# Kernel tuning notes

Hardware: AMD Instinct MI355X
Metric: run time of the kernel (lower is better)

## Reference

```python
import jax, jax.numpy as jnp
import numpy as np

B, NS, NF, T, D = 64, 2, 13, 24, 512
H = 8
DH = D // H
DFF = 2048
EPS = 1e-5


def setup_inputs() -> dict:
    key = jax.random.key(0)
    ks = jax.random.split(key, 16)
    s = 0.02
    inp = {
        'x': jax.random.normal(ks[0], (B, NS * NF, T, D), jnp.float32),
        'w_in_s': jax.random.normal(ks[1], (3 * D, D), jnp.float32) * s,
        'b_in_s': jnp.zeros((3 * D,), jnp.float32),
        'w_out_s': jax.random.normal(ks[2], (D, D), jnp.float32) * s,
        'b_out_s': jnp.zeros((D,), jnp.float32),
        'w_in_f': jax.random.normal(ks[3], (3 * D, D), jnp.float32) * s,
        'b_in_f': jnp.zeros((3 * D,), jnp.float32),
        'w_out_f': jax.random.normal(ks[4], (D, D), jnp.float32) * s,
        'b_out_f': jnp.zeros((D,), jnp.float32),
        'w1': jax.random.normal(ks[5], (DFF, D), jnp.float32) * s,
        'b1': jnp.zeros((DFF,), jnp.float32),
        'w2': jax.random.normal(ks[6], (D, DFF), jnp.float32) * s,
        'b2': jnp.zeros((D,), jnp.float32),
        'g1': jnp.ones((D,), jnp.float32), 'be1': jnp.zeros((D,), jnp.float32),
        'g2': jnp.ones((D,), jnp.float32), 'be2': jnp.zeros((D,), jnp.float32),
        'g3': jnp.ones((D,), jnp.float32), 'be3': jnp.zeros((D,), jnp.float32),
    }
    return inp


def _layer_norm(x, g, b):
    mu = jnp.mean(x, axis=-1, keepdims=True)
    var = jnp.mean(jnp.square(x - mu), axis=-1, keepdims=True)
    return (x - mu) * jax.lax.rsqrt(var + EPS) * g + b


def _mha(x, w_in, b_in, w_out, b_out):
    # x: [..., S, D]; torch nn.MultiheadAttention math, eval mode (no dropout)
    qkv = x @ w_in.T + b_in                     # [..., S, 3D]
    q, k, v = jnp.split(qkv, 3, axis=-1)
    shp = q.shape[:-1] + (H, DH)
    q, k, v = q.reshape(shp), k.reshape(shp), v.reshape(shp)
    scores = jnp.einsum('...qhd,...khd->...hqk', q, k) / np.sqrt(DH).astype(np.float32)
    a = jax.nn.softmax(scores, axis=-1)
    o = jnp.einsum('...hqk,...khd->...qhd', a, v).reshape(x.shape)
    return o @ w_out.T + b_out


def reference(x, w_in_s, b_in_s, w_out_s, b_out_s, w_in_f, b_in_f, w_out_f, b_out_f,
              w1, b1, w2, b2, g1, be1, g2, be2, g3, be3):
    xr = x.reshape(B, NS, NF, T, D)
    # station attention: attend over the NS axis for each (feature, t)
    xs = xr.transpose(0, 2, 3, 1, 4)            # [B, NF, T, NS, D]
    xs = xs + _mha(xs, w_in_s, b_in_s, w_out_s, b_out_s)
    x = xs.transpose(0, 3, 1, 2, 4).reshape(B, NS * NF, T, D)
    x = _layer_norm(x, g1, be1)
    # feature attention: attend over the NF axis for each (station, t)
    xr = x.reshape(B, NS, NF, T, D)
    xf = xr.transpose(0, 1, 3, 2, 4)            # [B, NS, T, NF, D]
    xf = xf + _mha(xf, w_in_f, b_in_f, w_out_f, b_out_f)
    x = xf.transpose(0, 1, 3, 2, 4).reshape(B, NS * NF, T, D)
    x = _layer_norm(x, g2, be2)
    # feed-forward
    ff = jax.nn.relu(x @ w1.T + b1) @ w2.T + b2
    x = _layer_norm(x + ff, g3, be3)
    return x
```

## Files before the change

kernel.cpp:

```cpp
#include <hip/hip_runtime.h>
#include <stdint.h>

typedef unsigned short u16;
typedef __bf16 bf16x8 __attribute__((ext_vector_type(8)));
typedef float f32x4 __attribute__((ext_vector_type(4)));

#define DEV __device__ __forceinline__

DEV float bf2f(u16 u) {
    union { uint32_t u; float f; } c; c.u = ((uint32_t)u) << 16; return c.f;
}
DEV u16 f2bf(float f) {
    union { float f; uint32_t u; } c; c.f = f;
    uint32_t u = c.u;
    u += 0x7FFFu + ((u >> 16) & 1u);
    return (u16)(u >> 16);
}

DEV void gload_lds16(const u16* gp, u16* lp) {
    __builtin_amdgcn_global_load_lds(
        (__attribute__((address_space(1))) u16*)(uintptr_t)gp,
        (__attribute__((address_space(3))) u16*)lp,
        16, 0, 0);
}

#define WAITVM6 asm volatile("s_waitcnt vmcnt(6)" ::: "memory")
#define WAITVM4 asm volatile("s_waitcnt vmcnt(4)" ::: "memory")
#define WAITVM0 asm volatile("s_waitcnt vmcnt(0)" ::: "memory")
#define MEMFENCE asm volatile("" ::: "memory")

DEV void load16f(const u16* p, float* f) {
    uint4 a = *reinterpret_cast<const uint4*>(p);
    uint4 b = *reinterpret_cast<const uint4*>(p + 8);
    uint32_t w[8] = { a.x, a.y, a.z, a.w, b.x, b.y, b.z, b.w };
#pragma unroll
    for (int k = 0; k < 8; ++k) {
        union { uint32_t u; float f; } lo, hi;
        lo.u = w[k] << 16; hi.u = w[k] & 0xFFFF0000u;
        f[2 * k] = lo.f; f[2 * k + 1] = hi.f;
    }
}
DEV float dot16(const u16* p, const float* q) {
    uint4 a = *reinterpret_cast<const uint4*>(p);
    uint4 b = *reinterpret_cast<const uint4*>(p + 8);
    uint32_t w[8] = { a.x, a.y, a.z, a.w, b.x, b.y, b.z, b.w };
    float d = 0.0f;
#pragma unroll
    for (int k = 0; k < 8; ++k) {
        union { uint32_t u; float f; } lo, hi;
        lo.u = w[k] << 16; hi.u = w[k] & 0xFFFF0000u;
        d += q[2 * k] * lo.f;
        d += q[2 * k + 1] * hi.f;
    }
    return d;
}
DEV void fma16(const u16* p, float pw, float* acc) {
    uint4 a = *reinterpret_cast<const uint4*>(p);
    uint4 b = *reinterpret_cast<const uint4*>(p + 8);
    uint32_t w[8] = { a.x, a.y, a.z, a.w, b.x, b.y, b.z, b.w };
#pragma unroll
    for (int k = 0; k < 8; ++k) {
        union { uint32_t u; float f; } lo, hi;
        lo.u = w[k] << 16; hi.u = w[k] & 0xFFFF0000u;
        acc[2 * k] += pw * lo.f;
        acc[2 * k + 1] += pw * hi.f;
    }
}
DEV void store16(u16* p, const float* y) {
    uint32_t w[8];
#pragma unroll
    for (int k = 0; k < 8; ++k)
        w[k] = (uint32_t)f2bf(y[2 * k]) | ((uint32_t)f2bf(y[2 * k + 1]) << 16);
    uint4 a = { w[0], w[1], w[2], w[3] };
    uint4 b = { w[4], w[5], w[6], w[7] };
    *reinterpret_cast<uint4*>(p) = a;
    *reinterpret_cast<uint4*>(p + 8) = b;
}

__global__ __launch_bounds__(256) void k_f32_to_bf16(
    const float* __restrict__ in, u16* __restrict__ out, int n4)
{
    int i = blockIdx.x * 256 + threadIdx.x;
    if (i >= n4) return;
    float4 v = reinterpret_cast<const float4*>(in)[i];
    ushort4 o;
    o.x = f2bf(v.x); o.y = f2bf(v.y); o.z = f2bf(v.z); o.w = f2bf(v.w);
    reinterpret_cast<ushort4*>(out)[i] = o;
}

template<bool RELU, bool RESID, int NT>
__global__ __launch_bounds__(512, 2) void k_gemm8p(
    const u16* __restrict__ A, const u16* __restrict__ W,
    const float* __restrict__ bias, const u16* __restrict__ res,
    u16* __restrict__ C, int M, int N, int K)
{
    __shared__ __align__(16) u16 Abuf[2][16384];
    __shared__ __align__(16) u16 Bbuf[2][16384];

    const int tid  = threadIdx.x;
    const int lane = tid & 63;
    const int wave = tid >> 6;
    const int wm   = wave >> 2;
    const int wn   = wave & 3;
    const int l15  = lane & 15;
    const int lg   = lane >> 4;

    const int nwg = gridDim.x;
    const int v = (blockIdx.x & 7) * (nwg >> 3) + (blockIdx.x >> 3);
    const long tileM = (long)(v / NT) * 256;
    const long tileN = (long)(v % NT) * 256;

    const int nIter = K >> 7;

    f32x4 acc[8][4] = {};

    const long Abase = (tileM + (tid >> 3)) * (long)K + (((tid & 7) ^ ((tid >> 3) & 7)) << 3);
    const long Bbase = (tileN + (tid >> 3)) * (long)K + (((tid & 7) ^ ((tid >> 3) & 7)) << 3);

    auto stA = [&](int h, int t) {
#pragma unroll
        for (int e = 0; e < 2; ++e)
            gload_lds16(A + Abase + (long)(h * 128 + e * 64) * K + t * 64,
                        &Abuf[t & 1][(h * 1024 + e * 512 + tid) * 8]);
    };
    auto stB = [&](int h, int t) {
#pragma unroll
        for (int e = 0; e < 2; ++e)
            gload_lds16(W + Bbase + (long)(h * 128 + e * 64) * K + t * 64,
                        &Bbuf[t & 1][(h * 1024 + e * 512 + tid) * 8]);
    };

    int koff[2];
#pragma unroll
    for (int ks = 0; ks < 2; ++ks)
        koff[ks] = ((ks * 4 + lg) ^ (l15 & 7)) * 8;
    const int aRow = wm * 128 + l15;
    const int bRow = wn * 64 + l15;

    stA(0, 0); stA(1, 0); stB(0, 0); stB(1, 0); stB(0, 1); stB(1, 1);
    WAITVM4;
    MEMFENCE;
    __builtin_amdgcn_s_barrier();
    MEMFENCE;

    bf16x8 b[4][2];

    for (int j = 0; j < nIter; ++j) {
        const bool pre = (j + 1 < nIter);
        const int E = 2 * j;
#pragma unroll
        for (int ph = 0; ph < 8; ++ph) {
            const int bb = ph >> 2;
            const int q  = ph & 3;
            if (q == 0) {
#pragma unroll
                for (int n = 0; n < 4; ++n)
#pragma unroll
                    for (int ks = 0; ks < 2; ++ks)
                        b[n][ks] = *reinterpret_cast<const bf16x8*>(
                            &Bbuf[bb][(bRow + n * 16) * 64 + koff[ks]]);
            }
            bf16x8 aq[2][2];
#pragma unroll
            for (int mi = 0; mi < 2; ++mi)
#pragma unroll
                for (int ks = 0; ks < 2; ++ks)
                    aq[mi][ks] = *reinterpret_cast<const bf16x8*>(
                        &Abuf[bb][(aRow + (q * 2 + mi) * 16) * 64 + koff[ks]]);
            if (ph == 0) stA(0, E + 1);
            else if (ph == 1) stA(1, E + 1);
            else if (ph == 2) { if (pre) stB(0, E + 2); }
            else if (ph == 3) {
                if (pre) { stB(1, E + 2); WAITVM4; } else { WAITVM0; }
            }
            else if (ph == 4) { if (pre) stA(0, E + 2); }
            else if (ph == 5) { if (pre) stA(1, E + 2); }
            else if (ph == 6) { if (pre) stB(0, E + 3); }
            else {
                if (pre) { stB(1, E + 3); WAITVM4; } else { WAITVM0; }
            }
            MEMFENCE;
            __builtin_amdgcn_s_barrier();
            MEMFENCE;
            __builtin_amdgcn_s_setprio(1);
#pragma unroll
            for (int mi = 0; mi < 2; ++mi)
#pragma unroll
                for (int n = 0; n < 4; ++n)
#pragma unroll
                    for (int ks = 0; ks < 2; ++ks)
                        acc[q * 2 + mi][n] = __builtin_amdgcn_mfma_f32_16x16x32_bf16(
                            aq[mi][ks], b[n][ks], acc[q * 2 + mi][n], 0, 0, 0);
            __builtin_amdgcn_s_setprio(0);
            MEMFENCE;
            __builtin_amdgcn_s_barrier();
            MEMFENCE;
        }
    }

    const int crow0 = (int)tileM + wm * 128 + ((lane >> 4) << 2);
    const int ccol0 = (int)tileN + wn * 64 + l15;
#pragma unroll
    for (int m = 0; m < 8; ++m) {
#pragma unroll
        for (int n = 0; n < 4; ++n) {
            const int col = ccol0 + n * 16;
            const float bv = bias[col];
#pragma unroll
            for (int r = 0; r < 4; ++r) {
                const long row = crow0 + m * 16 + r;
                float vv = acc[m][n][r] + bv;
                if (RESID) vv += bf2f(res[row * N + col]);
                if (RELU)  vv = fmaxf(vv, 0.0f);
                C[row * N + col] = f2bf(vv);
            }
        }
    }
}

template<bool RELU, bool RESID, int NT>
__global__ __launch_bounds__(512, 2) void k_gemm3s(
    const u16* __restrict__ A, const u16* __restrict__ W,
    const float* __restrict__ bias, const u16* __restrict__ res,
    u16* __restrict__ C, int M, int N, int K)
{
    __shared__ __align__(16) u16 Abuf[3][16384];
    __shared__ __align__(16) u16 Bbuf[3][8192];

    const int tid  = threadIdx.x;
    const int lane = tid & 63;
    const int wave = tid >> 6;
    const int wm   = wave >> 1;
    const int wn   = wave & 1;
    const int l15  = lane & 15;
    const int lg   = lane >> 4;

    const int nwg = gridDim.x;
    const int v = (blockIdx.x & 7) * (nwg >> 3) + (blockIdx.x >> 3);
    const long tileM = (long)(v / NT) * 256;
    const long tileN = (long)(v % NT) * 128;

    const int nT = K >> 6;

    f32x4 acc[4][4] = {};

    const long Abase = (tileM + (tid >> 3)) * (long)K + (((tid & 7) ^ ((tid >> 3) & 7)) << 3);
    const long Bbase = (tileN + (tid >> 3)) * (long)K + (((tid & 7) ^ ((tid >> 3) & 7)) << 3);

    auto stage = [&](int t, int p) {
        const int s = t % 3;
        const long ko = (long)t * 64;
        if (p == 0) {
#pragma unroll
            for (int e = 0; e < 3; ++e)
                gload_lds16(A + Abase + (long)(e * 64) * K + ko,
                            &Abuf[s][(e * 512 + tid) * 8]);
        } else {
            gload_lds16(A + Abase + (long)192 * K + ko,
                        &Abuf[s][(3 * 512 + tid) * 8]);
#pragma unroll
            for (int e = 0; e < 2; ++e)
                gload_lds16(W + Bbase + (long)(e * 64) * K + ko,
                            &Bbuf[s][(e * 512 + tid) * 8]);
        }
    };

    int koff[2];
#pragma unroll
    for (int ks = 0; ks < 2; ++ks)
        koff[ks] = ((ks * 4 + lg) ^ (l15 & 7)) * 8;
    const int aRow = wm * 64 + l15;
    const int bRow = wn * 64 + l15;

    stage(0, 0); stage(0, 1);
    stage(1, 0); stage(1, 1);
    WAITVM6;
    MEMFENCE;
    __builtin_amdgcn_s_barrier();
    MEMFENCE;

    for (int j = 0; j < nT; ++j) {
        const int s = j % 3;
        const u16* ab = Abuf[s];
        const u16* bb = Bbuf[s];
        const bool pre = (j + 2 < nT);

        bf16x8 bfr[4][2];
#pragma unroll
        for (int n = 0; n < 4; ++n)
#pragma unroll
            for (int ks = 0; ks < 2; ++ks)
                bfr[n][ks] = *reinterpret_cast<const bf16x8*>(
                    &bb[(bRow + n * 16) * 64 + koff[ks]]);
        bf16x8 a0[2][2];
#pragma unroll
        for (int mi = 0; mi < 2; ++mi)
#pragma unroll
            for (int ks = 0; ks < 2; ++ks)
                a0[mi][ks] = *reinterpret_cast<const bf16x8*>(
                    &ab[(aRow + mi * 16) * 64 + koff[ks]]);
        if (pre) stage(j + 2, 0);
        MEMFENCE;
        __builtin_amdgcn_s_barrier();
        MEMFENCE;
        __builtin_amdgcn_s_setprio(1);
#pragma unroll
        for (int mi = 0; mi < 2; ++mi)
#pragma unroll
            for (int n = 0; n < 4; ++n)
#pragma unroll
                for (int ks = 0; ks < 2; ++ks)
                    acc[mi][n] = __builtin_amdgcn_mfma_f32_16x16x32_bf16(
                        a0[mi][ks], bfr[n][ks], acc[mi][n], 0, 0, 0);
        __builtin_amdgcn_s_setprio(0);
        MEMFENCE;
        __builtin_amdgcn_s_barrier();
        MEMFENCE;

        bf16x8 a1[2][2];
#pragma unroll
        for (int mi = 0; mi < 2; ++mi)
#pragma unroll
            for (int ks = 0; ks < 2; ++ks)
                a1[mi][ks] = *reinterpret_cast<const bf16x8*>(
                    &ab[(aRow + (2 + mi) * 16) * 64 + koff[ks]]);
        if (pre) { stage(j + 2, 1); WAITVM6; }
        else if (j + 1 < nT) { WAITVM0; }
        MEMFENCE;
        __builtin_amdgcn_s_barrier();
        MEMFENCE;
        __builtin_amdgcn_s_setprio(1);
#pragma unroll
        for (int mi = 0; mi < 2; ++mi)
#pragma unroll
            for (int n = 0; n < 4; ++n)
#pragma unroll
                for (int ks = 0; ks < 2; ++ks)
                    acc[2 + mi][n] = __builtin_amdgcn_mfma_f32_16x16x32_bf16(
                        a1[mi][ks], bfr[n][ks], acc[2 + mi][n], 0, 0, 0);
        __builtin_amdgcn_s_setprio(0);
        MEMFENCE;
        __builtin_amdgcn_s_barrier();
        MEMFENCE;
    }

    const int crow0 = (int)tileM + wm * 64 + ((lane >> 4) << 2);
    const int ccol0 = (int)tileN + wn * 64 + l15;
#pragma unroll
    for (int m = 0; m < 4; ++m) {
#pragma unroll
        for (int n = 0; n < 4; ++n) {
            const int col = ccol0 + n * 16;
            const float bv = bias[col];
#pragma unroll
            for (int r = 0; r < 4; ++r) {
                const long row = crow0 + m * 16 + r;
                float vv = acc[m][n][r] + bv;
                if (RESID) vv += bf2f(res[row * N + col]);
                if (RELU)  vv = fmaxf(vv, 0.0f);
                C[row * N + col] = f2bf(vv);
            }
        }
    }
}

__global__ __launch_bounds__(256) void k_attn_s(
    const u16* __restrict__ qkv, u16* __restrict__ o)
{
    const int wave = threadIdx.x >> 6, lane = threadIdx.x & 63;
    const int g = blockIdx.x * 4 + wave;
    const int t = g % 24, bf = g / 24, f = bf % 13, b = bf / 13;
    const int base = b * 624 + f * 24 + t;
    const int h = lane >> 3, i = (lane >> 2) & 1, c = lane & 3;
    const int off = h * 64 + c * 16;

    float qf[16];
    load16f(qkv + (size_t)(base + i * 312) * 1536 + off, qf);

    float s[2];
#pragma unroll
    for (int j = 0; j < 2; ++j) {
        float d = dot16(qkv + (size_t)(base + j * 312) * 1536 + 512 + off, qf);
        d += __shfl_xor(d, 1);
        d += __shfl_xor(d, 2);
        s[j] = d * 0.125f;
    }
    const float m = fmaxf(s[0], s[1]);
    const float e0 = expf(s[0] - m), e1 = expf(s[1] - m);
    const float inv = 1.0f / (e0 + e1);
    const float p0 = e0 * inv, p1 = e1 * inv;

    float acc[16] = {};
    fma16(qkv + (size_t)base * 1536 + 1024 + off, p0, acc);
    fma16(qkv + (size_t)(base + 312) * 1536 + 1024 + off, p1, acc);

    store16(o + (size_t)(base + i * 312) * 512 + off, acc);
}

__global__ __launch_bounds__(256) void k_attn_f(
    const u16* __restrict__ qkv, u16* __restrict__ o)
{
    const int wave = threadIdx.x >> 6, lane = threadIdx.x & 63;
    const int p = blockIdx.x * 4 + wave;
    const int h = p & 7, g = p >> 3;
    const int t = g % 24, bs = g / 24, st = bs % 2, b = bs / 2;
    const int base = b * 624 + st * 312 + t;
    const int i = lane >> 2, c = lane & 3;
    const int iq = (i < 13) ? i : 12;
    const int off = h * 64 + c * 16;

    float qf[16];
    load16f(qkv + (size_t)(base + iq * 24) * 1536 + off, qf);

    float sc[13];
#pragma unroll
    for (int j = 0; j < 13; ++j) {
        float d = dot16(qkv + (size_t)(base + j * 24) * 1536 + 512 + off, qf);
        d += __shfl_xor(d, 1);
        d += __shfl_xor(d, 2);
        sc[j] = d * 0.125f;
    }
    float m = sc[0];
#pragma unroll
    for (int j = 1; j < 13; ++j) m = fmaxf(m, sc[j]);
    float den = 0.0f;
#pragma unroll
    for (int j = 0; j < 13; ++j) { sc[j] = expf(sc[j] - m); den += sc[j]; }
    const float inv = 1.0f / den;

    float acc[16] = {};
#pragma unroll
    for (int j = 0; j < 13; ++j)
        fma16(qkv + (size_t)(base + j * 24) * 1536 + 1024 + off, sc[j], acc);
#pragma unroll
    for (int e = 0; e < 16; ++e) acc[e] *= inv;

    if (i < 13)
        store16(o + (size_t)(base + i * 24) * 512 + off, acc);
}

template<bool OUTF32>
__global__ __launch_bounds__(256) void k_ln(
    const u16* __restrict__ in, const float* __restrict__ g,
    const float* __restrict__ be, u16* __restrict__ outb,
    float* __restrict__ outf)
{
    const int row  = blockIdx.x * 4 + (threadIdx.x >> 6);
    const int lane = threadIdx.x & 63;
    const u16* p = in + (size_t)row * 512 + lane * 8;

    uint4 va = *reinterpret_cast<const uint4*>(p);
    uint32_t ua[4] = { va.x, va.y, va.z, va.w };
    float x[8];
#pragma unroll
    for (int i = 0; i < 4; ++i) {
        x[2 * i]     = bf2f((u16)(ua[i] & 0xFFFFu));
        x[2 * i + 1] = bf2f((u16)(ua[i] >> 16));
    }
    float s = 0.f, sq = 0.f;
#pragma unroll
    for (int i = 0; i < 8; ++i) { s += x[i]; sq += x[i] * x[i]; }
#pragma unroll
    for (int off = 32; off; off >>= 1) {
        s  += __shfl_xor(s, off);
        sq += __shfl_xor(sq, off);
    }
    const float mean = s * (1.0f / 512.0f);
    const float var  = sq * (1.0f / 512.0f) - mean * mean;
    const float rstd = rsqrtf(var + 1e-5f);

    const int col = lane * 8;
    float4 g0 = *reinterpret_cast<const float4*>(g + col);
    float4 g1 = *reinterpret_cast<const float4*>(g + col + 4);
    float4 b0 = *reinterpret_cast<const float4*>(be + col);
    float4 b1 = *reinterpret_cast<const float4*>(be + col + 4);
    float gg[8] = { g0.x, g0.y, g0.z, g0.w, g1.x, g1.y, g1.z, g1.w };
    float bb[8] = { b0.x, b0.y, b0.z, b0.w, b1.x, b1.y, b1.z, b1.w };

    float y[8];
#pragma unroll
    for (int i = 0; i < 8; ++i) y[i] = (x[i] - mean) * rstd * gg[i] + bb[i];

    if (OUTF32) {
        float4 o0 = { y[0], y[1], y[2], y[3] };
        float4 o1 = { y[4], y[5], y[6], y[7] };
        reinterpret_cast<float4*>(outf + (size_t)row * 512 + col)[0] = o0;
        reinterpret_cast<float4*>(outf + (size_t)row * 512 + col + 4)[0] = o1;
    } else {
        uint32_t w[4];
#pragma unroll
        for (int i = 0; i < 4; ++i)
            w[i] = (uint32_t)f2bf(y[2 * i]) | ((uint32_t)f2bf(y[2 * i + 1]) << 16);
        uint4 ov = { w[0], w[1], w[2], w[3] };
        *reinterpret_cast<uint4*>(outb + (size_t)row * 512 + col) = ov;
    }
}

extern "C" void kernel_launch(void* const* d_in, const int* in_sizes, int n_in,
                              void* d_out, int out_size, void* d_ws, size_t ws_size,
                              hipStream_t stream)
{
    const float* x       = (const float*)d_in[0];
    const float* w_in_s  = (const float*)d_in[1];
    const float* b_in_s  = (const float*)d_in[2];
    const float* w_out_s = (const float*)d_in[3];
    const float* b_out_s = (const float*)d_in[4];
    const float* w_in_f  = (const float*)d_in[5];
    const float* b_in_f  = (const float*)d_in[6];
    const float* w_out_f = (const float*)d_in[7];
    const float* b_out_f = (const float*)d_in[8];
    const float* w1      = (const float*)d_in[9];
    const float* b1      = (const float*)d_in[10];
    const float* w2      = (const float*)d_in[11];
    const float* b2      = (const float*)d_in[12];
    const float* g1      = (const float*)d_in[13];
    const float* be1     = (const float*)d_in[14];
    const float* g2      = (const float*)d_in[15];
    const float* be2     = (const float*)d_in[16];
    const float* g3      = (const float*)d_in[17];
    const float* be3     = (const float*)d_in[18];

    const int R = 39936;
    u16* xb   = (u16*)d_ws;
    u16* buf1 = xb + (size_t)R * 512;
    u16* obuf = buf1 + (size_t)R * 1536;
    u16* wqs  = buf1 + (size_t)R * 2048;
    u16* wos  = wqs + 1536 * 512;
    u16* wqf  = wos + 512 * 512;
    u16* wof  = wqf + 1536 * 512;
    u16* w1b  = wof + 512 * 512;
    u16* w2b  = w1b + 2048 * 512;

    auto conv = [&](const float* src, u16* dst, int n) {
        int n4 = n / 4;
        k_f32_to_bf16<<<dim3((n4 + 255) / 256), dim3(256), 0, stream>>>(src, dst, n4);
    };
    conv(x,       xb,  R * 512);
    conv(w_in_s,  wqs, 1536 * 512);
    conv(w_out_s, wos, 512 * 512);
    conv(w_in_f,  wqf, 1536 * 512);
    conv(w_out_f, wof, 512 * 512);
    conv(w1,      w1b, 2048 * 512);
    conv(w2,      w2b, 512 * 2048);

    const dim3 blk256(256);
    const dim3 blk512(512);

    k_gemm8p<false, false, 6><<<dim3(936), blk512, 0, stream>>>(
        xb, wqs, b_in_s, nullptr, buf1, R, 1536, 512);
    k_attn_s<<<dim3(19968 / 4), blk256, 0, stream>>>(buf1, obuf);
    k_gemm3s<false, true, 4><<<dim3(624), blk512, 0, stream>>>(
        obuf, wos, b_out_s, xb, xb, R, 512, 512);
    k_ln<false><<<dim3(R / 4), blk256, 0, stream>>>(xb, g1, be1, xb, nullptr);

    k_gemm8p<false, false, 6><<<dim3(936), blk512, 0, stream>>>(
        xb, wqf, b_in_f, nullptr, buf1, R, 1536, 512);
    k_attn_f<<<dim3(24576 / 4), blk256, 0, stream>>>(buf1, obuf);
    k_gemm3s<false, true, 4><<<dim3(624), blk512, 0, stream>>>(
        obuf, wof, b_out_f, xb, xb, R, 512, 512);
    k_ln<false><<<dim3(R / 4), blk256, 0, stream>>>(xb, g2, be2, xb, nullptr);

    k_gemm8p<true, false, 8><<<dim3(1248), blk512, 0, stream>>>(
        xb, w1b, b1, nullptr, buf1, R, 2048, 512);
    k_gemm3s<false, true, 4><<<dim3(624), blk512, 0, stream>>>(
        buf1, w2b, b2, xb, xb, R, 512, 2048);
    k_ln<true><<<dim3(R / 4), blk256, 0, stream>>>(xb, g3, be3, nullptr, (float*)d_out);
}
```

Baseline: 623.9 us.

## Fuse station QKV projection with two-token station attention in one kernel

```diff
diff --git a/kernel.cpp b/kernel.cpp
--- a/kernel.cpp
+++ b/kernel.cpp
@@ -28,6 +28,13 @@
 #define WAITVM4 asm volatile("s_waitcnt vmcnt(4)" ::: "memory")
 #define WAITVM0 asm volatile("s_waitcnt vmcnt(0)" ::: "memory")
 #define MEMFENCE asm volatile("" ::: "memory")
+
+DEV int phys_row(int L) {
+    const int s = L & 1, T = L >> 1;
+    const int t = T % 24, F = T / 24;
+    const int f = F % 13, b = F / 13;
+    return b * 624 + s * 312 + f * 24 + t;
+}
 
 DEV void load16f(const u16* p, float* f) {
     uint4 a = *reinterpret_cast<const uint4*>(p);
@@ -88,6 +95,127 @@
     reinterpret_cast<ushort4*>(out)[i] = o;
 }
 
+__global__ __launch_bounds__(256) void k_qkva(
+    const u16* __restrict__ A, const u16* __restrict__ W,
+    const float* __restrict__ bias, u16* __restrict__ O)
+{
+    __shared__ __align__(16) u16 As[2][4096];
+    __shared__ __align__(16) u16 Bs[2][6144];
+
+    const int tid  = threadIdx.x;
+    const int lane = tid & 63;
+    const int wave = tid >> 6;
+    const int l15  = lane & 15;
+    const int lg   = lane >> 4;
+
+    const int bid = blockIdx.x;
+    const int v = (bid & 7) * 312 + (bid >> 3);
+    const int mtile = v >> 3;
+    const int head  = v & 7;
+    const int Lb = mtile * 128;
+
+    f32x4 acc[2][12] = {};
+
+    const int srow = tid >> 2;
+    const int c8 = ((tid & 3) ^ ((tid >> 3) & 3)) * 8;
+    const long pa0 = (long)phys_row(Lb + srow) * 512 + c8;
+    const long pa1 = (long)phys_row(Lb + srow + 64) * 512 + c8;
+    long pb[3];
+#pragma unroll
+    for (int e = 0; e < 3; ++e) {
+        const int r = srow + e * 64;
+        pb[e] = (long)((r >> 6) * 512 + head * 64 + (r & 63)) * 512 + c8;
+    }
+    const int dst0 = wave * 512;
+
+    auto stage = [&](int buf, int kk) {
+        gload_lds16(A + pa0 + kk, &As[buf][dst0]);
+        gload_lds16(A + pa1 + kk, &As[buf][2048 + dst0]);
+        gload_lds16(W + pb[0] + kk, &Bs[buf][dst0]);
+        gload_lds16(W + pb[1] + kk, &Bs[buf][2048 + dst0]);
+        gload_lds16(W + pb[2] + kk, &Bs[buf][4096 + dst0]);
+    };
+    const int koff = ((lane >> 4) ^ ((lane >> 1) & 3)) * 8;
+    auto compute = [&](int buf) {
+        bf16x8 b[12], a[2];
+#pragma unroll
+        for (int n = 0; n < 12; ++n)
+            b[n] = *reinterpret_cast<const bf16x8*>(&Bs[buf][(n * 16 + l15) * 32 + koff]);
+#pragma unroll
+        for (int m = 0; m < 2; ++m)
+            a[m] = *reinterpret_cast<const bf16x8*>(&As[buf][(wave * 32 + m * 16 + l15) * 32 + koff]);
+#pragma unroll
+        for (int m = 0; m < 2; ++m)
+#pragma unroll
+            for (int n = 0; n < 12; ++n)
+                acc[m][n] = __builtin_amdgcn_mfma_f32_16x16x32_bf16(
+                    a[m], b[n], acc[m][n], 0, 0, 0);
+    };
+
+    stage(0, 0);
+    __syncthreads();
+    int cur = 0;
+    for (int kk = 0; kk < 512 - 32; kk += 32) {
+        stage(cur ^ 1, kk + 32);
+        compute(cur);
+        __syncthreads();
+        cur ^= 1;
+    }
+    compute(cur);
+
+    float bv[12];
+#pragma unroll
+    for (int n = 0; n < 12; ++n)
+        bv[n] = bias[(n >> 2) * 512 + head * 64 + l15 + 16 * (n & 3)];
+#pragma unroll
+    for (int m = 0; m < 2; ++m)
+#pragma unroll
+        for (int n = 0; n < 12; ++n)
+#pragma unroll
+            for (int r = 0; r < 4; ++r) acc[m][n][r] += bv[n];
+
+#pragma unroll
+    for (int m = 0; m < 2; ++m) {
+        int prow[4];
+#pragma unroll
+        for (int r = 0; r < 4; ++r)
+            prow[r] = phys_row(Lb + wave * 32 + m * 16 + 4 * lg + r);
+#pragma unroll
+        for (int p = 0; p < 2; ++p) {
+            float s00 = 0.f, s01 = 0.f, s10 = 0.f, s11 = 0.f;
+#pragma unroll
+            for (int n = 0; n < 4; ++n) {
+                const float q0 = acc[m][n][2 * p],     q1 = acc[m][n][2 * p + 1];
+                const float k0 = acc[m][4 + n][2 * p], k1 = acc[m][4 + n][2 * p + 1];
+                s00 += q0 * k0; s01 += q0 * k1; s10 += q1 * k0; s11 += q1 * k1;
+            }
+#pragma unroll
+            for (int e = 1; e < 16; e <<= 1) {
+                s00 += __shfl_xor(s00, e);
+                s01 += __shfl_xor(s01, e);
+                s10 += __shfl_xor(s10, e);
+                s11 += __shfl_xor(s11, e);
+            }
+            s00 *= 0.125f; s01 *= 0.125f; s10 *= 0.125f; s11 *= 0.125f;
+            const float m0 = fmaxf(s00, s01), m1 = fmaxf(s10, s11);
+            const float e00 = expf(s00 - m0), e01 = expf(s01 - m0);
+            const float e10 = expf(s10 - m1), e11 = expf(s11 - m1);
+            const float i0 = 1.0f / (e00 + e01), i1 = 1.0f / (e10 + e11);
+            const float p00 = e00 * i0, p01 = e01 * i0;
+            const float p10 = e10 * i1, p11 = e11 * i1;
+            const long r0 = (long)prow[2 * p] * 512 + head * 64 + l15;
+            const long r1 = (long)prow[2 * p + 1] * 512 + head * 64 + l15;
+#pragma unroll
+            for (int n = 0; n < 4; ++n) {
+                const float v0 = acc[m][8 + n][2 * p];
+                const float v1 = acc[m][8 + n][2 * p + 1];
+                O[r0 + 16 * n] = f2bf(p00 * v0 + p01 * v1);
+                O[r1 + 16 * n] = f2bf(p10 * v0 + p11 * v1);
+            }
+        }
+    }
+}
+
 template<bool RELU, bool RESID, int NT>
 __global__ __launch_bounds__(512, 2) void k_gemm8p(
     const u16* __restrict__ A, const u16* __restrict__ W,
@@ -362,39 +490,6 @@
             }
         }
     }
-}
-
-__global__ __launch_bounds__(256) void k_attn_s(
-    const u16* __restrict__ qkv, u16* __restrict__ o)
-{
-    const int wave = threadIdx.x >> 6, lane = threadIdx.x & 63;
-    const int g = blockIdx.x * 4 + wave;
-    const int t = g % 24, bf = g / 24, f = bf % 13, b = bf / 13;
-    const int base = b * 624 + f * 24 + t;
-    const int h = lane >> 3, i = (lane >> 2) & 1, c = lane & 3;
-    const int off = h * 64 + c * 16;
-
-    float qf[16];
-    load16f(qkv + (size_t)(base + i * 312) * 1536 + off, qf);
-
-    float s[2];
-#pragma unroll
-    for (int j = 0; j < 2; ++j) {
-        float d = dot16(qkv + (size_t)(base + j * 312) * 1536 + 512 + off, qf);
-        d += __shfl_xor(d, 1);
-        d += __shfl_xor(d, 2);
-        s[j] = d * 0.125f;
-    }
-    const float m = fmaxf(s[0], s[1]);
-    const float e0 = expf(s[0] - m), e1 = expf(s[1] - m);
-    const float inv = 1.0f / (e0 + e1);
-    const float p0 = e0 * inv, p1 = e1 * inv;
-
-    float acc[16] = {};
-    fma16(qkv + (size_t)base * 1536 + 1024 + off, p0, acc);
-    fma16(qkv + (size_t)(base + 312) * 1536 + 1024 + off, p1, acc);
-
-    store16(o + (size_t)(base + i * 312) * 512 + off, acc);
 }
 
 __global__ __launch_bounds__(256) void k_attn_f(
@@ -546,9 +641,7 @@
     const dim3 blk256(256);
     const dim3 blk512(512);
 
-    k_gemm8p<false, false, 6><<<dim3(936), blk512, 0, stream>>>(
-        xb, wqs, b_in_s, nullptr, buf1, R, 1536, 512);
-    k_attn_s<<<dim3(19968 / 4), blk256, 0, stream>>>(buf1, obuf);
+    k_qkva<<<dim3(2496), blk256, 0, stream>>>(xb, wqs, b_in_s, obuf);
     k_gemm3s<false, true, 4><<<dim3(624), blk512, 0, stream>>>(
         obuf, wos, b_out_s, xb, xb, R, 512, 512);
     k_ln<false><<<dim3(R / 4), blk256, 0, stream>>>(xb, g1, be1, xb, nullptr);
```

Result: slower. 645.7 us (+3.5%).
